# Kernel optimization log

Hardware: AMD Instinct MI355X
Metric: run time of the kernel (lower is better)

## Reference

```python
import jax, jax.numpy as jnp
from jax import lax
import numpy as np

PROPRIO = 48
NPTS = 1024
NP_PROX = 512
NP_DIST = 512
HP = 187  # proximal_feature_dim
HD = 64   # distal_feature_dim
B = 2048
NA = 12
ACTOR_DIMS = [PROPRIO + HP + HD, 1024, 512, 256, 128, NA]


def gru_last(x, wih, whh, bih, bhh):
    """torch-style GRU (gate order r,z,n), returns last hidden. x: [B,T,in]."""
    Bx, T, _ = x.shape
    H = whh.shape[1]
    gx = x @ wih.T + bih  # [B,T,3H], input projections precomputed
    def step(h, gxt):
        gh = h @ whh.T + bhh
        r = jax.nn.sigmoid(gxt[:, :H] + gh[:, :H])
        z = jax.nn.sigmoid(gxt[:, H:2 * H] + gh[:, H:2 * H])
        n = jnp.tanh(gxt[:, 2 * H:] + r * gh[:, 2 * H:])
        return (1.0 - z) * n + z * h, None
    h0 = jnp.zeros((Bx, H), x.dtype)
    hT, _ = lax.scan(step, h0, jnp.swapaxes(gx, 0, 1))
    return hT


def _encode(pts, w1, b1, w2, b2):
    h = jax.nn.elu(pts @ w1.T + b1)
    return jax.nn.elu(h @ w2.T + b2)


def _forward(obs, pe_prox_w1, pe_prox_b1, pe_prox_w2, pe_prox_b2,
             pe_dist_w1, pe_dist_b1, pe_dist_w2, pe_dist_b2,
             gru_prox_wih, gru_prox_whh, gru_prox_bih, gru_prox_bhh,
             gru_dist_wih, gru_dist_whh, gru_dist_bih, gru_dist_bhh,
             mem_prox_wih, mem_prox_whh, mem_prox_bih, mem_prox_bhh,
             mem_dist_wih, mem_dist_whh, mem_dist_bih, mem_dist_bhh,
             actor_w0, actor_b0, actor_w1, actor_b1, actor_w2, actor_b2,
             actor_w3, actor_b3, actor_w4, actor_b4,
             prox_idx, dist_idx):
    proprio = obs[:, :PROPRIO]
    lidar = obs[:, PROPRIO:].reshape(obs.shape[0], NPTS, 3)  # history_length=1
    # irregular gather of proximal/distal point subsets (sampling plan buffers)
    prox_enc = _encode(lidar[:, prox_idx], pe_prox_w1, pe_prox_b1, pe_prox_w2, pe_prox_b2)  # [B,512,64]
    dist_enc = _encode(lidar[:, dist_idx], pe_dist_w1, pe_dist_b1, pe_dist_w2, pe_dist_b2)  # [B,512,64]
    # spatial GRUs over the point sequence
    hp = gru_last(prox_enc, gru_prox_wih, gru_prox_whh, gru_prox_bih, gru_prox_bhh)  # [B,187]
    hd = gru_last(dist_enc, gru_dist_wih, gru_dist_whh, gru_dist_bih, gru_dist_bhh)  # [B,64]
    # temporal memory GRUs (single step, zero initial hidden)
    fp = gru_last(hp[:, None, :], mem_prox_wih, mem_prox_whh, mem_prox_bih, mem_prox_bhh)
    fd = gru_last(hd[:, None, :], mem_dist_wih, mem_dist_whh, mem_dist_bih, mem_dist_bhh)
    x = jnp.concatenate([proprio, fp, fd], axis=-1)  # [B,299]
    for w, b in ((actor_w0, actor_b0), (actor_w1, actor_b1), (actor_w2, actor_b2), (actor_w3, actor_b3)):
        x = jax.nn.elu(x @ w.T + b)
    return x @ actor_w4.T + actor_b4  # action mean [B,12]


def setup_inputs() -> dict:
    key = jax.random.key(0)
    ks = iter(jax.random.split(key, 64))
    def n(shape, scale=0.05):
        return (jax.random.normal(next(ks), shape, jnp.float32) * scale)
    inp = {}
    inp["obs"] = jax.random.normal(next(ks), (B, PROPRIO + NPTS * 3), jnp.float32)
    inp["prox_idx"] = jax.random.randint(next(ks), (NP_PROX,), 0, NPTS)
    inp["dist_idx"] = jax.random.randint(next(ks), (NP_DIST,), 0, NPTS)
    for pfx in ("pe_prox", "pe_dist"):
        inp[pfx + "_w1"] = n((64, 3)); inp[pfx + "_b1"] = jnp.zeros((64,), jnp.float32)
        inp[pfx + "_w2"] = n((64, 64)); inp[pfx + "_b2"] = jnp.zeros((64,), jnp.float32)
    for pfx, H, din in (("gru_prox", HP, 64), ("gru_dist", HD, 64), ("mem_prox", HP, HP), ("mem_dist", HD, HD)):
        inp[pfx + "_wih"] = n((3 * H, din)); inp[pfx + "_whh"] = n((3 * H, H))
        inp[pfx + "_bih"] = jnp.zeros((3 * H,), jnp.float32); inp[pfx + "_bhh"] = jnp.zeros((3 * H,), jnp.float32)
    for i, (di, do) in enumerate(zip(ACTOR_DIMS[:-1], ACTOR_DIMS[1:])):
        inp[f"actor_w{i}"] = n((do, di)); inp[f"actor_b{i}"] = jnp.zeros((do,), jnp.float32)
    return inp


def reference(obs, prox_idx, dist_idx,
              pe_prox_w1, pe_prox_b1, pe_prox_w2, pe_prox_b2,
              pe_dist_w1, pe_dist_b1, pe_dist_w2, pe_dist_b2,
              gru_prox_wih, gru_prox_whh, gru_prox_bih, gru_prox_bhh,
              gru_dist_wih, gru_dist_whh, gru_dist_bih, gru_dist_bhh,
              mem_prox_wih, mem_prox_whh, mem_prox_bih, mem_prox_bhh,
              mem_dist_wih, mem_dist_whh, mem_dist_bih, mem_dist_bhh,
              actor_w0, actor_b0, actor_w1, actor_b1, actor_w2, actor_b2,
              actor_w3, actor_b3, actor_w4, actor_b4):
    return _forward(obs, pe_prox_w1, pe_prox_b1, pe_prox_w2, pe_prox_b2,
                    pe_dist_w1, pe_dist_b1, pe_dist_w2, pe_dist_b2,
                    gru_prox_wih, gru_prox_whh, gru_prox_bih, gru_prox_bhh,
                    gru_dist_wih, gru_dist_whh, gru_dist_bih, gru_dist_bhh,
                    mem_prox_wih, mem_prox_whh, mem_prox_bih, mem_prox_bhh,
                    mem_dist_wih, mem_dist_whh, mem_dist_bih, mem_dist_bhh,
                    actor_w0, actor_b0, actor_w1, actor_b1, actor_w2, actor_b2,
                    actor_w3, actor_b3, actor_w4, actor_b4,
                    prox_idx, dist_idx)
```

## Files before the change

kernel.cpp:

```cpp
#include <hip/hip_runtime.h>
#include <stdint.h>

typedef __attribute__((ext_vector_type(8))) short short8;
typedef __attribute__((ext_vector_type(4))) float f32x4;
typedef __attribute__((ext_vector_type(4))) unsigned int u32x4;

#define DEV __device__ __forceinline__

#define L2E 1.4426950408889634f

DEV unsigned short f2bf(float f) {
    union { float f; uint32_t u; } v; v.f = f;
    return (unsigned short)((v.u + 0x7FFFu + ((v.u >> 16) & 1u)) >> 16);
}
#if defined(__has_builtin)
#if __has_builtin(__builtin_amdgcn_cvt_pk_bf16_f32)
#define HAS_PK_BF16 1
#endif
#endif
DEV uint32_t pk_bf16(float a, float b) {
#ifdef HAS_PK_BF16
    typedef __attribute__((ext_vector_type(2))) __bf16 bf2;
    union { bf2 v; uint32_t u; } cv;
    cv.v = __builtin_amdgcn_cvt_pk_bf16_f32(a, b);
    return cv.u;
#else
    return (uint32_t)f2bf(a) | ((uint32_t)f2bf(b) << 16);
#endif
}
DEV uint8_t f2fp8(float f) {
    union { float f; uint32_t u; } v; v.f = f;
    uint32_t s = (v.u >> 24) & 0x80u;
    uint32_t absu = v.u & 0x7FFFFFFFu;
    int E = (int)(absu >> 23);
    if (E >= 136) return (uint8_t)(s | 0x7E);
    if (E >= 121) {
        uint32_t m = absu & 0x7FFFFFu;
        uint32_t keep = m >> 20;
        uint32_t rest = m & 0xFFFFFu;
        uint32_t rnd = (rest > 0x80000u || (rest == 0x80000u && (keep & 1u))) ? 1u : 0u;
        uint32_t mag = (((uint32_t)(E - 120) << 3) | keep) + rnd;
        if (mag > 0x7Eu) mag = 0x7Eu;
        return (uint8_t)(s | mag);
    }
    float sc = __builtin_fabsf(f) * 512.f;
    uint32_t m8 = (uint32_t)(sc + 0.5f);
    if (m8 > 7u) return (uint8_t)(s | 0x08);
    return (uint8_t)(s | m8);
}
DEV float rcp1pe_(float x) {
    return __builtin_amdgcn_rcpf(1.f + __builtin_amdgcn_exp2f(x));
}
DEV float sig_(float x) { return rcp1pe_(-L2E * x); }
DEV float elu_(float x) {
    return x > 0.f ? x : __builtin_amdgcn_exp2f(L2E * x) - 1.f;
}
DEV f32x4 splat4(float v) { f32x4 r; r[0]=v; r[1]=v; r[2]=v; r[3]=v; return r; }
DEV void pin(short8& v) { asm volatile("" : "+v"(v)); }
DEV void pinl(long& v)  { asm volatile("" : "+v"(v)); }

struct PJob { const float* s; void* d; int Hs, NG, Ks, Kd, total; float s0, s1, s2; int fmt; };
struct PJobs { PJob j[13]; };

__global__ __launch_bounds__(256) void pack_all(PJobs P)
{
    PJob jb = P.j[blockIdx.y];
    int e = blockIdx.x * 256 + threadIdx.x;
    if (e >= jb.total) return;
    int n = e / jb.Kd, k = e - n * jb.Kd;
    int g = n / jb.NG, jj = n - g * jb.NG;
    float sc = (g == 0) ? jb.s0 : ((g == 1) ? jb.s1 : jb.s2);
    float v = (jj < jb.Hs && k < jb.Ks) ? jb.s[(size_t)(g * jb.Hs + jj) * jb.Ks + k] * sc : 0.f;
    if (jb.fmt) ((uint8_t*)jb.d)[e] = f2fp8(v);
    else        ((unsigned short*)jb.d)[e] = f2bf(v);
}

__global__ __launch_bounds__(256) void enc_kernel(
    const float* __restrict__ obs, const int* __restrict__ idx,
    const float* __restrict__ w1, const float* __restrict__ b1,
    const unsigned short* __restrict__ w2p, const float* __restrict__ b2,
    uint8_t* __restrict__ enc8)
{
    const int b = blockIdx.x, t0 = blockIdx.y * 64;
    const int tid = threadIdx.x;
    __shared__ __align__(16) float pts[64][4];
    __shared__ float w1s[256];
    __shared__ float b1s[64], b2s[64];
    __shared__ __align__(16) unsigned short h1s[64][72];

    if (tid < 192) w1s[(tid/3)*4 + (tid - (tid/3)*3)] = w1[tid];
    if (tid < 64) { b1s[tid] = b1[tid]; b2s[tid] = b2[tid]; }
    for (int e = tid; e < 192; e += 256) {
        int p = e / 3, c2 = e - p * 3;
        int pi = idx[t0 + p];
        pts[p][c2] = obs[(size_t)b * 3120 + 48 + (size_t)pi * 3 + c2];
    }
    __syncthreads();
#pragma unroll
    for (int r = 0; r < 16; ++r) {
        int e = tid + r * 256;
        int p = e >> 6, ch = e & 63;
        float v = w1s[ch*4]*pts[p][0] + w1s[ch*4+1]*pts[p][1]
                + w1s[ch*4+2]*pts[p][2] + b1s[ch];
        h1s[p][ch] = f2bf(elu_(v));
    }
    __syncthreads();
    const int wave = tid >> 6, lane = tid & 63, quad = lane >> 4, l16 = lane & 15;
#pragma unroll
    for (int ct = 0; ct < 4; ++ct) {
        f32x4 a2 = splat4(0.f);
#pragma unroll
        for (int ks = 0; ks < 2; ++ks) {
            short8 af = *(const short8*)(&h1s[wave*16 + l16][ks*32 + quad*8]);
            short8 bf = *(const short8*)(w2p + (ct*16 + l16)*64 + ks*32 + quad*8);
            a2 = __builtin_amdgcn_mfma_f32_16x16x32_bf16(af, bf, a2, 0, 0, 0);
        }
        int c = ct*16 + l16;
        float b2v = b2s[c];
#pragma unroll
        for (int j = 0; j < 4; ++j) {
            int m = wave*16 + quad*4 + j;
            enc8[((size_t)b*512 + t0 + m)*64 + c] = f2fp8(elu_(a2[j] + b2v));
        }
    }
}

DEV void gru_body_pre(int blk, const uint8_t* __restrict__ enc8,
                      const uint8_t* __restrict__ wih8,
                      const unsigned short* __restrict__ whh,
                      const float* __restrict__ bih, const float* __restrict__ bhh,
                      unsigned short* __restrict__ houtb, char* smem)
{
    constexpr int H = 187, KP = 192, KS = 6, HP8 = 200;
    unsigned short* hlds = (unsigned short*)smem;
    uint8_t* xs = (uint8_t*)(smem + 12800);

    const int tid  = threadIdx.x;
    const int wave = tid >> 6, lane = tid & 63, quad = lane >> 4, l16 = lane & 15;
    const int b0   = blk * 16;
    const int c    = wave * 16 + l16;

    for (int e = tid; e < 2*16*HP8; e += 768) hlds[e] = 0;

    short8 whr[3][KS];
    long   wx8[3][2];
#pragma unroll
    for (int g = 0; g < 3; ++g) {
#pragma unroll
        for (int ks = 0; ks < KS; ++ks)
            whr[g][ks] = *(const short8*)(whh + ((size_t)(g*KP + c))*KP + ks*32 + quad*8);
#pragma unroll
        for (int ks = 0; ks < 2; ++ks)
            wx8[g][ks] = *(const long*)(wih8 + ((size_t)(g*KP + c))*64 + ks*32 + quad*8);
    }
#pragma unroll
    for (int g = 0; g < 3; ++g) {
#pragma unroll
        for (int ks = 0; ks < KS; ++ks) pin(whr[g][ks]);
#pragma unroll
        for (int ks = 0; ks < 2; ++ks)  pinl(wx8[g][ks]);
    }
    float bsr = 0.f, bsz = 0.f, binx = 0.f, bhnn = 0.f;
    if (c < H) {
        bsr  = -L2E * (bih[c]       + bhh[c]);
        bsz  = -L2E * (bih[H + c]   + bhh[H + c]);
        binx = 2.f * L2E * bih[2*H + c];
        bhnn = 2.f * L2E * bhh[2*H + c];
    }
    float hreg[4] = {0.f, 0.f, 0.f, 0.f};

    u32x4 xq;
    const int xrow = lane >> 2, xseg = lane & 3;
    if (wave == 0) {
        xq = *(const u32x4*)(enc8 + ((size_t)(b0 + xrow)*512 + 0)*64 + xseg*16);
        *(u32x4*)(xs + 0*1280 + xrow*80 + xseg*16) = xq;
        xq = *(const u32x4*)(enc8 + ((size_t)(b0 + xrow)*512 + 1)*64 + xseg*16);
    }
    __syncthreads();

    int cur = 0;
    for (int t = 0; t < 512; ++t) {
        if (wave == 0) {
            *(u32x4*)(xs + ((t+1)&1)*1280 + xrow*80 + xseg*16) = xq;
            int tn = (t + 2 < 512) ? t + 2 : 511;
            xq = *(const u32x4*)(enc8 + ((size_t)(b0 + xrow)*512 + tn)*64 + xseg*16);
        }
        const uint8_t* xsr = xs + (t&1)*1280;
        const unsigned short* hc = hlds + cur * (16*HP8);
        unsigned short*       hn = hlds + (cur ^ 1) * (16*HP8);

        f32x4 acc[4];
        acc[0] = splat4(bsr);
        acc[1] = splat4(bsz);
        acc[2] = splat4(binx);
        acc[3] = splat4(bhnn);
#pragma unroll
        for (int ks = 0; ks < 2; ++ks) {
            long a8 = *(const long*)(xsr + l16*80 + ks*32 + quad*8);
            acc[0] = __builtin_amdgcn_mfma_f32_16x16x32_fp8_fp8(a8, wx8[0][ks], acc[0], 0, 0, 0);
            acc[1] = __builtin_amdgcn_mfma_f32_16x16x32_fp8_fp8(a8, wx8[1][ks], acc[1], 0, 0, 0);
            acc[2] = __builtin_amdgcn_mfma_f32_16x16x32_fp8_fp8(a8, wx8[2][ks], acc[2], 0, 0, 0);
        }
#pragma unroll
        for (int ks = 0; ks < KS; ++ks) {
            short8 ah = *(const short8*)(hc + l16*HP8 + ks*32 + quad*8);
            acc[0] = __builtin_amdgcn_mfma_f32_16x16x32_bf16(ah, whr[0][ks], acc[0], 0, 0, 0);
            acc[1] = __builtin_amdgcn_mfma_f32_16x16x32_bf16(ah, whr[1][ks], acc[1], 0, 0, 0);
            acc[3] = __builtin_amdgcn_mfma_f32_16x16x32_bf16(ah, whr[2][ks], acc[3], 0, 0, 0);
        }
        float hv[4];
#pragma unroll
        for (int j = 0; j < 4; ++j) {
            float r  = rcp1pe_(acc[0][j]);
            float zg = rcp1pe_(acc[1][j]);
            float nn = __builtin_fmaf(-2.f, rcp1pe_(__builtin_fmaf(r, acc[3][j], acc[2][j])), 1.f);
            hv[j] = __builtin_fmaf(zg, hreg[j] - nn, nn);
            hreg[j] = hv[j];
        }
        uint32_t p01 = pk_bf16(hv[0], hv[1]);
        uint32_t p23 = pk_bf16(hv[2], hv[3]);
        hn[(quad*4+0)*HP8 + c] = (unsigned short)p01;
        hn[(quad*4+1)*HP8 + c] = (unsigned short)(p01 >> 16);
        hn[(quad*4+2)*HP8 + c] = (unsigned short)p23;
        hn[(quad*4+3)*HP8 + c] = (unsigned short)(p23 >> 16);
        cur ^= 1;
        __syncthreads();
    }
#pragma unroll
    for (int j = 0; j < 4; ++j) {
        int m = quad*4 + j;
        houtb[(size_t)(b0 + m)*KP + c] = (c < H) ? f2bf(hreg[j]) : 0;
    }
}

template<int H, int KP>
DEV void gru_body_fused(int blk,
                  const float* __restrict__ obs, const int* __restrict__ idx,
                  const float* __restrict__ w1, const float* __restrict__ b1,
                  const float* __restrict__ w2, const float* __restrict__ b2,
                  const unsigned short* __restrict__ wih, const unsigned short* __restrict__ whh,
                  const float* __restrict__ bih, const float* __restrict__ bhh,
                  unsigned short* __restrict__ houtb, char* smem)
{
    constexpr int NCT = KP / 16;
    constexpr int KS  = KP / 32;
    constexpr int HP8 = KP + 8;

    unsigned short* hlds = (unsigned short*)(smem);
    unsigned short* xs   = (unsigned short*)(smem + 12800);
    unsigned short* h1s  = (unsigned short*)(smem + 17408);
    unsigned short* w2s  = (unsigned short*)(smem + 22016);
    float* ptsb          = (float*)(smem + 31232);
    float* w1s           = (float*)(smem + 31744);
    float* b1s           = (float*)(smem + 32768);
    float* b2s           = (float*)(smem + 33024);

    const int tid  = threadIdx.x;
    const int wave = tid >> 6, lane = tid & 63, quad = lane >> 4, l16 = lane & 15;
    const int b0   = blk * 16;
    const int ct   = wave;
    const bool act = (ct < NCT);
    const int c    = ct * 16 + l16;

    for (int e = tid; e < 2*16*HP8; e += 768) hlds[e] = 0;
    for (int e = tid; e < 4096; e += 768) { int n = e >> 6, k = e & 63; w2s[n*72 + k] = f2bf(w2[e]); }
    if (tid < 192) w1s[(tid/3)*4 + (tid - (tid/3)*3)] = w1[tid];
    if (tid < 64) { b1s[tid] = b1[tid]; b2s[tid] = b2[tid]; }

    const float* myrow = obs + (size_t)(b0 + (tid & 15)) * 3120 + 48;
    float px = 0.f, py = 0.f, pz = 0.f;
    if (tid < 16) {
        int p0 = idx[0];
        ptsb[tid*4 + 0] = myrow[3*p0 + 0];
        ptsb[tid*4 + 1] = myrow[3*p0 + 1];
        ptsb[tid*4 + 2] = myrow[3*p0 + 2];
        int p1 = idx[1];
        px = myrow[3*p1 + 0]; py = myrow[3*p1 + 1]; pz = myrow[3*p1 + 2];
    }

    short8 whr[3][KS];
    short8 wxr[3][2];
    float bsr = 0.f, bsz = 0.f, binx = 0.f, bhnn = 0.f;
    {
        const int cl = act ? c : l16;
#pragma unroll
        for (int g = 0; g < 3; ++g) {
#pragma unroll
            for (int ks = 0; ks < KS; ++ks)
                whr[g][ks] = *(const short8*)(whh + ((size_t)(g*KP + cl))*KP + ks*32 + quad*8);
#pragma unroll
            for (int ks = 0; ks < 2; ++ks)
                wxr[g][ks] = *(const short8*)(wih + ((size_t)(g*KP + cl))*64 + ks*32 + quad*8);
        }
    }
#pragma unroll
    for (int g = 0; g < 3; ++g) {
#pragma unroll
        for (int ks = 0; ks < KS; ++ks) pin(whr[g][ks]);
#pragma unroll
        for (int ks = 0; ks < 2; ++ks)  pin(wxr[g][ks]);
    }
    if (act && c < H) {
        bsr  = -L2E * (bih[c]       + bhh[c]);
        bsz  = -L2E * (bih[H + c]   + bhh[H + c]);
        binx = 2.f * L2E * bih[2*H + c];
        bhnn = 2.f * L2E * bhh[2*H + c];
    }
    float hreg[4] = {0.f, 0.f, 0.f, 0.f};

    __syncthreads();

    int cur = 0;
    for (int i = 0; i < 514; ++i) {
        if (i < 512) {
            const float* pt = ptsb + (i & 1) * 64;
            unsigned short* h1w = h1s + (i & 1) * (16*72);
#pragma unroll
            for (int e = tid; e < 1024; e += 768) {
                int p = e >> 6, ch = e & 63;
                float v = w1s[ch*4+0]*pt[p*4+0] + w1s[ch*4+1]*pt[p*4+1]
                        + w1s[ch*4+2]*pt[p*4+2] + b1s[ch];
                h1w[p*72 + ch] = f2bf(elu_(v));
            }
            if (tid < 16) {
                float* dst = ptsb + ((i+1) & 1) * 64 + tid*4;
                dst[0] = px; dst[1] = py; dst[2] = pz;
                int tn = (i + 2 < 512) ? i + 2 : 511;
                int pn = idx[tn];
                px = myrow[3*pn + 0]; py = myrow[3*pn + 1]; pz = myrow[3*pn + 2];
            }
        }
        if (i >= 1 && i < 513 && wave < 4) {
            const unsigned short* h1r = h1s + ((i-1) & 1) * (16*72);
            unsigned short*       xw  = xs  + ((i-1) & 1) * (16*72);
            f32x4 a2 = splat4(0.f);
#pragma unroll
            for (int ks = 0; ks < 2; ++ks) {
                short8 af = *(const short8*)(h1r + l16*72 + ks*32 + quad*8);
                short8 bf = *(const short8*)(w2s + (wave*16 + l16)*72 + ks*32 + quad*8);
                a2 = __builtin_amdgcn_mfma_f32_16x16x32_bf16(af, bf, a2, 0, 0, 0);
            }
            int c2 = wave*16 + l16;
            float b2v = b2s[c2];
#pragma unroll
            for (int j = 0; j < 4; ++j)
                xw[(quad*4 + j)*72 + c2] = f2bf(elu_(a2[j] + b2v));
        }
        if (i >= 2) {
            int t = i - 2;
            const unsigned short* xsr = xs + (t & 1) * (16*72);
            const unsigned short* hc  = hlds + cur * (16*HP8);
            unsigned short*       hn  = hlds + (cur ^ 1) * (16*HP8);
            if (act) {
                f32x4 acc[4];
                acc[0] = splat4(bsr);
                acc[1] = splat4(bsz);
                acc[2] = splat4(binx);
                acc[3] = splat4(bhnn);
#pragma unroll
                for (int ks = 0; ks < 2; ++ks) {
                    short8 xf = *(const short8*)(xsr + l16*72 + ks*32 + quad*8);
                    acc[0] = __builtin_amdgcn_mfma_f32_16x16x32_bf16(xf, wxr[0][ks], acc[0], 0, 0, 0);
                    acc[1] = __builtin_amdgcn_mfma_f32_16x16x32_bf16(xf, wxr[1][ks], acc[1], 0, 0, 0);
                    acc[2] = __builtin_amdgcn_mfma_f32_16x16x32_bf16(xf, wxr[2][ks], acc[2], 0, 0, 0);
                }
#pragma unroll
                for (int ks = 0; ks < KS; ++ks) {
                    short8 ah = *(const short8*)(hc + l16*HP8 + ks*32 + quad*8);
                    acc[0] = __builtin_amdgcn_mfma_f32_16x16x32_bf16(ah, whr[0][ks], acc[0], 0, 0, 0);
                    acc[1] = __builtin_amdgcn_mfma_f32_16x16x32_bf16(ah, whr[1][ks], acc[1], 0, 0, 0);
                    acc[3] = __builtin_amdgcn_mfma_f32_16x16x32_bf16(ah, whr[2][ks], acc[3], 0, 0, 0);
                }
                float hv[4];
#pragma unroll
                for (int j = 0; j < 4; ++j) {
                    float r  = rcp1pe_(acc[0][j]);
                    float zg = rcp1pe_(acc[1][j]);
                    float nn = __builtin_fmaf(-2.f, rcp1pe_(__builtin_fmaf(r, acc[3][j], acc[2][j])), 1.f);
                    hv[j] = __builtin_fmaf(zg, hreg[j] - nn, nn);
                    hreg[j] = hv[j];
                }
                uint32_t p01 = pk_bf16(hv[0], hv[1]);
                uint32_t p23 = pk_bf16(hv[2], hv[3]);
                hn[(quad*4+0)*HP8 + c] = (unsigned short)p01;
                hn[(quad*4+1)*HP8 + c] = (unsigned short)(p01 >> 16);
                hn[(quad*4+2)*HP8 + c] = (unsigned short)p23;
                hn[(quad*4+3)*HP8 + c] = (unsigned short)(p23 >> 16);
            }
            cur ^= 1;
        }
        __syncthreads();
    }

    if (act)
#pragma unroll
        for (int j = 0; j < 4; ++j) {
            int m = quad*4 + j;
            houtb[(size_t)(b0 + m)*KP + c] = (c < H) ? f2bf(hreg[j]) : 0;
        }
}

__global__ __launch_bounds__(768) void gru_kernel(
    int mode,
    const float* __restrict__ obs,
    const int* __restrict__ prox_idx, const int* __restrict__ dist_idx,
    const uint8_t* __restrict__ encp8, const uint8_t* __restrict__ wihp8,
    const float* __restrict__ w1p, const float* __restrict__ b1p,
    const float* __restrict__ w2p, const float* __restrict__ b2p,
    const float* __restrict__ w1d, const float* __restrict__ b1d,
    const float* __restrict__ w2d, const float* __restrict__ b2d,
    const unsigned short* __restrict__ wihp, const unsigned short* __restrict__ whhp,
    const unsigned short* __restrict__ wihd, const unsigned short* __restrict__ whhd,
    const float* __restrict__ bihp, const float* __restrict__ bhhp,
    const float* __restrict__ bihd, const float* __restrict__ bhhd,
    unsigned short* __restrict__ hpb, unsigned short* __restrict__ hdb)
{
    __shared__ __align__(16) char smem[33280];
    if (blockIdx.x < 128) {
        if (mode == 0)
            gru_body_pre(blockIdx.x, encp8, wihp8, whhp, bihp, bhhp, hpb, smem);
        else
            gru_body_fused<187, 192>(blockIdx.x, obs, prox_idx, w1p, b1p, w2p, b2p,
                                     wihp, whhp, bihp, bhhp, hpb, smem);
    } else {
        gru_body_fused<64, 64>(blockIdx.x - 128, obs, dist_idx, w1d, b1d, w2d, b2d,
                               wihd, whhd, bihd, bhhd, hdb, smem);
    }
}

__global__ __launch_bounds__(256) void memfuse_kernel(
    const float* __restrict__ obs,
    const unsigned short* __restrict__ hpb, const unsigned short* __restrict__ hdb,
    const unsigned short* __restrict__ mwp, const unsigned short* __restrict__ mwd,
    const float* __restrict__ mbip, const float* __restrict__ mbhp,
    const float* __restrict__ mbid, const float* __restrict__ mbhd,
    unsigned short* __restrict__ x0b)
{
    __shared__ __align__(16) unsigned short Asl[64*40];
    __shared__ __align__(16) unsigned short Bsl[3][64*40];
    const int tid = threadIdx.x;
    const int wave = tid >> 6, lane = tid & 63, quad = lane >> 4, l16 = lane & 15;
    const int z = blockIdx.x, m0 = blockIdx.y * 64;
    const bool isp = (z < 3);
    const unsigned short* A = isp ? hpb : hdb;
    const unsigned short* B = isp ? mwp : mwd;
    const float* bi = isp ? mbip : mbid;
    const float* bh = isp ? mbhp : mbhd;
    const int Kp = isp ? 192 : 64;
    const int Hh = isp ? 187 : 64;
    const int jb = isp ? z * 64 : 0;
    const int cbase = isp ? 48 : 235;
    const int r = tid >> 2, sg = (tid & 3) * 8;

    f32x4 acc[3][4];
#pragma unroll
    for (int g = 0; g < 3; ++g)
#pragma unroll
        for (int nt = 0; nt < 4; ++nt) acc[g][nt] = splat4(0.f);

    for (int k0 = 0; k0 < Kp; k0 += 32) {
        *(short8*)(Asl + r*40 + sg) = *(const short8*)(A + (size_t)(m0 + r)*Kp + k0 + sg);
#pragma unroll
        for (int g = 0; g < 3; ++g)
            *(short8*)(Bsl[g] + r*40 + sg) =
                *(const short8*)(B + (size_t)(g*Kp + jb + r)*Kp + k0 + sg);
        __syncthreads();
        short8 af = *(const short8*)(Asl + (wave*16 + l16)*40 + quad*8);
#pragma unroll
        for (int g = 0; g < 3; ++g)
#pragma unroll
            for (int nt = 0; nt < 4; ++nt) {
                short8 bf = *(const short8*)(Bsl[g] + (nt*16 + l16)*40 + quad*8);
                acc[g][nt] = __builtin_amdgcn_mfma_f32_16x16x32_bf16(af, bf, acc[g][nt], 0, 0, 0);
            }
        __syncthreads();
    }
#pragma unroll
    for (int nt = 0; nt < 4; ++nt) {
        int j = jb + nt*16 + l16;
        bool valid = (j < Hh);
        float br = 0.f, bz = 0.f, bnx = 0.f, bnh = 0.f;
        if (valid) {
            br  = -L2E * (bi[j] + bh[j]);
            bz  = -L2E * (bi[Hh + j] + bh[Hh + j]);
            bnx = 2.f * L2E * bi[2*Hh + j];
            bnh = 2.f * L2E * bh[2*Hh + j];
        }
#pragma unroll
        for (int jj = 0; jj < 4; ++jj) {
            int m = m0 + wave*16 + quad*4 + jj;
            float rr = rcp1pe_(acc[0][nt][jj] + br);
            float zz = rcp1pe_(acc[1][nt][jj] + bz);
            float tt = __builtin_fmaf(rr, bnh, acc[2][nt][jj] + bnx);
            float nn = __builtin_fmaf(-2.f, rcp1pe_(tt), 1.f);
            float v  = (1.f - zz) * nn;
            if (valid) x0b[(size_t)m*320 + cbase + j] = f2bf(v);
        }
    }
    if (z == 0) {
        for (int e = tid; e < 64*48; e += 256) {
            int m = m0 + e / 48, cc = e - (e / 48) * 48;
            x0b[(size_t)m*320 + cc] = f2bf(obs[(size_t)m*3120 + cc]);
        }
    }
    if (z == 3) {
        for (int e = tid; e < 64*21; e += 256) {
            int m = m0 + e / 21, cc = 299 + (e - (e / 21) * 21);
            x0b[(size_t)m*320 + cc] = 0;
        }
    }
}

__global__ __launch_bounds__(256) void bgemm_kernel(
    const unsigned short* __restrict__ A, const unsigned short* __restrict__ B,
    const float* __restrict__ bias, void* __restrict__ C,
    int Kp, int Np, int Nstore, int mode)
{
    __shared__ __align__(16) unsigned short Asl[64*40];
    __shared__ __align__(16) unsigned short Bsl[64*40];
    const int tid = threadIdx.x;
    const int wave = tid >> 6, lane = tid & 63, quad = lane >> 4, l16 = lane & 15;
    const int n0 = blockIdx.x * 64, m0 = blockIdx.y * 64;
    const int r = tid >> 2, sg = (tid & 3) * 8;

    f32x4 acc[4];
#pragma unroll
    for (int nt = 0; nt < 4; ++nt) acc[nt] = splat4(0.f);

    for (int k0 = 0; k0 < Kp; k0 += 32) {
        short8 av = *(const short8*)(A + (size_t)(m0 + r)*Kp + k0 + sg);
        short8 bv;
        if (n0 + r < Np) bv = *(const short8*)(B + (size_t)(n0 + r)*Kp + k0 + sg);
        else { short8 zz; for (int q = 0; q < 8; ++q) zz[q] = 0; bv = zz; }
        *(short8*)(Asl + r*40 + sg) = av;
        *(short8*)(Bsl + r*40 + sg) = bv;
        __syncthreads();
        short8 af = *(const short8*)(Asl + (wave*16 + l16)*40 + quad*8);
#pragma unroll
        for (int nt = 0; nt < 4; ++nt) {
            short8 bf = *(const short8*)(Bsl + (nt*16 + l16)*40 + quad*8);
            acc[nt] = __builtin_amdgcn_mfma_f32_16x16x32_bf16(af, bf, acc[nt], 0, 0, 0);
        }
        __syncthreads();
    }
#pragma unroll
    for (int nt = 0; nt < 4; ++nt) {
        int n = n0 + nt*16 + l16;
        float bv = (bias && n < Np) ? bias[n] : 0.f;
#pragma unroll
        for (int j = 0; j < 4; ++j) {
            int m = m0 + wave*16 + quad*4 + j;
            float v = acc[nt][j] + bv;
            if (mode == 1) {
                ((unsigned short*)C)[(size_t)m*Np + n] = f2bf(elu_(v));
            } else {
                if (n < Nstore) ((float*)C)[(size_t)m*Nstore + n] = v;
            }
        }
    }
}

extern "C" void kernel_launch(void* const* d_in, const int* in_sizes, int n_in,
                              void* d_out, int out_size, void* d_ws, size_t ws_size,
                              hipStream_t stream)
{
    (void)in_sizes; (void)n_in; (void)out_size;
    const float* obs        = (const float*)d_in[0];
    const int*   prox_idx   = (const int*)d_in[1];
    const int*   dist_idx   = (const int*)d_in[2];
    const float* pe_prox_w1 = (const float*)d_in[3];
    const float* pe_prox_b1 = (const float*)d_in[4];
    const float* pe_prox_w2 = (const float*)d_in[5];
    const float* pe_prox_b2 = (const float*)d_in[6];
    const float* pe_dist_w1 = (const float*)d_in[7];
    const float* pe_dist_b1 = (const float*)d_in[8];
    const float* pe_dist_w2 = (const float*)d_in[9];
    const float* pe_dist_b2 = (const float*)d_in[10];
    const float* gp_wih = (const float*)d_in[11];
    const float* gp_whh = (const float*)d_in[12];
    const float* gp_bih = (const float*)d_in[13];
    const float* gp_bhh = (const float*)d_in[14];
    const float* gd_wih = (const float*)d_in[15];
    const float* gd_whh = (const float*)d_in[16];
    const float* gd_bih = (const float*)d_in[17];
    const float* gd_bhh = (const float*)d_in[18];
    const float* mp_wih = (const float*)d_in[19];
    const float* mp_bih = (const float*)d_in[21];
    const float* mp_bhh = (const float*)d_in[22];
    const float* md_wih = (const float*)d_in[23];
    const float* md_bih = (const float*)d_in[25];
    const float* md_bhh = (const float*)d_in[26];
    const float* aw0 = (const float*)d_in[27]; const float* ab0 = (const float*)d_in[28];
    const float* aw1 = (const float*)d_in[29]; const float* ab1 = (const float*)d_in[30];
    const float* aw2 = (const float*)d_in[31]; const float* ab2 = (const float*)d_in[32];
    const float* aw3 = (const float*)d_in[33]; const float* ab3 = (const float*)d_in[34];
    const float* aw4 = (const float*)d_in[35]; const float* ab4 = (const float*)d_in[36];
    float* out = (float*)d_out;

    char* ws = (char*)d_ws;
    size_t off = 0;
    auto alloc = [&](size_t bytes) -> char* {
        char* p = ws + off;
        off = (off + bytes + 255) & ~(size_t)255;
        return p;
    };
    unsigned short* wih_p = (unsigned short*)alloc(36864*2);
    unsigned short* whh_p = (unsigned short*)alloc(110592*2);
    unsigned short* wih_d = (unsigned short*)alloc(12288*2);
    unsigned short* whh_d = (unsigned short*)alloc(12288*2);
    unsigned short* mw_p  = (unsigned short*)alloc(110592*2);
    unsigned short* mw_d  = (unsigned short*)alloc(12288*2);
    unsigned short* w0p   = (unsigned short*)alloc((size_t)1024*320*2);
    unsigned short* w1p   = (unsigned short*)alloc((size_t)512*1024*2);
    unsigned short* w2p   = (unsigned short*)alloc((size_t)256*512*2);
    unsigned short* w3p   = (unsigned short*)alloc((size_t)128*256*2);
    unsigned short* w4p   = (unsigned short*)alloc((size_t)16*128*2);
    unsigned short* w2e   = (unsigned short*)alloc(4096*2);
    uint8_t* wih8         = (uint8_t*)alloc(576*64);
    unsigned short* hpb   = (unsigned short*)alloc((size_t)2048*192*2);
    unsigned short* hdb   = (unsigned short*)alloc((size_t)2048*64*2);
    unsigned short* x0b   = (unsigned short*)alloc((size_t)2048*320*2);
    unsigned short* a1b   = (unsigned short*)alloc((size_t)2048*1024*2);
    unsigned short* a2b   = (unsigned short*)alloc((size_t)2048*512*2);
    unsigned short* a3b   = (unsigned short*)alloc((size_t)2048*256*2);
    unsigned short* a4b   = (unsigned short*)alloc((size_t)2048*128*2);
    uint8_t* enc8         = (uint8_t*)alloc((size_t)2048*512*64);
    const int mode = (off <= ws_size) ? 0 : 1;

    const float SR = -L2E, SN = 2.f * L2E;
    PJobs P;
    P.j[0]  = { gp_wih, wih_p, 187, 192, 64, 64, 36864, SR, SR, SN, 0 };
    P.j[1]  = { gp_whh, whh_p, 187, 192, 187, 192, 110592, SR, SR, SN, 0 };
    P.j[2]  = { gd_wih, wih_d, 64, 64, 64, 64, 12288, SR, SR, SN, 0 };
    P.j[3]  = { gd_whh, whh_d, 64, 64, 64, 64, 12288, SR, SR, SN, 0 };
    P.j[4]  = { mp_wih, mw_p, 187, 192, 187, 192, 110592, SR, SR, SN, 0 };
    P.j[5]  = { md_wih, mw_d, 64, 64, 64, 64, 12288, SR, SR, SN, 0 };
    P.j[6]  = { aw0, w0p, 1024, 1024, 299, 320, 327680, 1.f, 1.f, 1.f, 0 };
    P.j[7]  = { aw1, w1p, 512, 512, 1024, 1024, 524288, 1.f, 1.f, 1.f, 0 };
    P.j[8]  = { aw2, w2p, 256, 256, 512, 512, 131072, 1.f, 1.f, 1.f, 0 };
    P.j[9]  = { aw3, w3p, 128, 128, 256, 256, 32768, 1.f, 1.f, 1.f, 0 };
    P.j[10] = { aw4, w4p, 12, 16, 128, 128, 2048, 1.f, 1.f, 1.f, 0 };
    P.j[11] = { pe_prox_w2, w2e, 64, 64, 64, 64, 4096, 1.f, 1.f, 1.f, 0 };
    P.j[12] = { gp_wih, wih8, 187, 192, 64, 64, 36864, SR, SR, SN, 1 };
    pack_all<<<dim3(2048, 13), 256, 0, stream>>>(P);

    if (mode == 0) {
        enc_kernel<<<dim3(2048, 8), 256, 0, stream>>>(
            obs, prox_idx, pe_prox_w1, pe_prox_b1, w2e, pe_prox_b2, enc8);
    }

    gru_kernel<<<256, 768, 0, stream>>>(
        mode, obs, prox_idx, dist_idx, enc8, wih8,
        pe_prox_w1, pe_prox_b1, pe_prox_w2, pe_prox_b2,
        pe_dist_w1, pe_dist_b1, pe_dist_w2, pe_dist_b2,
        wih_p, whh_p, wih_d, whh_d,
        gp_bih, gp_bhh, gd_bih, gd_bhh, hpb, hdb);

    memfuse_kernel<<<dim3(4, 32), 256, 0, stream>>>(
        obs, hpb, hdb, mw_p, mw_d, mp_bih, mp_bhh, md_bih, md_bhh, x0b);

    bgemm_kernel<<<dim3(16, 32), 256, 0, stream>>>(x0b, w0p, ab0, a1b, 320, 1024, 1024, 1);
    bgemm_kernel<<<dim3(8,  32), 256, 0, stream>>>(a1b, w1p, ab1, a2b, 1024, 512, 512, 1);
    bgemm_kernel<<<dim3(4,  32), 256, 0, stream>>>(a2b, w2p, ab2, a3b, 512, 256, 256, 1);
    bgemm_kernel<<<dim3(2,  32), 256, 0, stream>>>(a3b, w3p, ab3, a4b, 256, 128, 128, 1);
    bgemm_kernel<<<dim3(1,  32), 256, 0, stream>>>(a4b, w4p, ab4, out, 128, 16, 12, 0);
}
```

Measured before the change: 811.0 us.

## Vectorize FP8 packing, swizzle GRU LDS, widen GEMM K-tile, fuse last two layers

Uses the hardware packed FP8 conversion and stages encoder outputs in shared memory so they can be written with 16-byte stores. Applies an XOR swizzle to the GRU hidden-state LDS layout to cut bank conflicts. Doubles the bgemm K step to 64 to halve the number of barriers. Fuses actor layers 3 and 4 into one kernel, which removes the a4 intermediate and one launch. The hardware FP8 conversion may round slightly differently from the software f2fp8, and the fused kernel runs only 32 blocks.

```diff
diff --git a/kernel.cpp b/kernel.cpp
--- a/kernel.cpp
+++ b/kernel.cpp
@@ -16,6 +16,9 @@
 #if defined(__has_builtin)
 #if __has_builtin(__builtin_amdgcn_cvt_pk_bf16_f32)
 #define HAS_PK_BF16 1
+#endif
+#if __has_builtin(__builtin_amdgcn_cvt_pk_fp8_f32)
+#define HAS_PK_FP8 1
 #endif
 #endif
 DEV uint32_t pk_bf16(float a, float b) {
@@ -48,6 +51,16 @@
     if (m8 > 7u) return (uint8_t)(s | 0x08);
     return (uint8_t)(s | m8);
 }
+DEV uint32_t pk_fp8x4(float a, float b, float c, float d) {
+#ifdef HAS_PK_FP8
+    int lo   = __builtin_amdgcn_cvt_pk_fp8_f32(a, b, 0, false);
+    int both = __builtin_amdgcn_cvt_pk_fp8_f32(c, d, lo, true);
+    return (uint32_t)both;
+#else
+    return (uint32_t)f2fp8(a) | ((uint32_t)f2fp8(b) << 8)
+         | ((uint32_t)f2fp8(c) << 16) | ((uint32_t)f2fp8(d) << 24);
+#endif
+}
 DEV float rcp1pe_(float x) {
     return __builtin_amdgcn_rcpf(1.f + __builtin_amdgcn_exp2f(x));
 }
@@ -71,7 +84,7 @@
     int g = n / jb.NG, jj = n - g * jb.NG;
     float sc = (g == 0) ? jb.s0 : ((g == 1) ? jb.s1 : jb.s2);
     float v = (jj < jb.Hs && k < jb.Ks) ? jb.s[(size_t)(g * jb.Hs + jj) * jb.Ks + k] * sc : 0.f;
-    if (jb.fmt) ((uint8_t*)jb.d)[e] = f2fp8(v);
+    if (jb.fmt) ((uint8_t*)jb.d)[e] = (uint8_t)(pk_fp8x4(v, 0.f, 0.f, 0.f) & 0xFFu);
     else        ((unsigned short*)jb.d)[e] = f2bf(v);
 }
 
@@ -87,6 +100,7 @@
     __shared__ float w1s[256];
     __shared__ float b1s[64], b2s[64];
     __shared__ __align__(16) unsigned short h1s[64][72];
+    __shared__ __align__(16) uint8_t x8s[64 * 80];
 
     if (tid < 192) w1s[(tid/3)*4 + (tid - (tid/3)*3)] = w1[tid];
     if (tid < 64) { b1s[tid] = b1[tid]; b2s[tid] = b2[tid]; }
@@ -117,11 +131,17 @@
         }
         int c = ct*16 + l16;
         float b2v = b2s[c];
-#pragma unroll
-        for (int j = 0; j < 4; ++j) {
-            int m = wave*16 + quad*4 + j;
-            enc8[((size_t)b*512 + t0 + m)*64 + c] = f2fp8(elu_(a2[j] + b2v));
-        }
+        uint32_t pk = pk_fp8x4(elu_(a2[0] + b2v), elu_(a2[1] + b2v),
+                               elu_(a2[2] + b2v), elu_(a2[3] + b2v));
+#pragma unroll
+        for (int j = 0; j < 4; ++j)
+            x8s[(wave*16 + quad*4 + j)*80 + c] = (uint8_t)(pk >> (8*j));
+    }
+    __syncthreads();
+    {
+        int row = tid >> 2, seg = tid & 3;
+        *(u32x4*)(enc8 + ((size_t)b*512 + t0 + row)*64 + seg*16) =
+            *(const u32x4*)(x8s + row*80 + seg*16);
     }
 }
 
@@ -139,6 +159,11 @@
     const int wave = tid >> 6, lane = tid & 63, quad = lane >> 4, l16 = lane & 15;
     const int b0   = blk * 16;
     const int c    = wave * 16 + l16;
+
+    const int sx = (l16 >> 2) & 3;
+    const int qo = (quad ^ sx) * 8;
+    const int cc = c >> 3, cl = c & 7;
+    const int wcol = ((cc & ~3) | ((cc & 3) ^ quad)) * 8 + cl;
 
     for (int e = tid; e < 2*16*HP8; e += 768) hlds[e] = 0;
 
@@ -203,7 +228,7 @@
         }
 #pragma unroll
         for (int ks = 0; ks < KS; ++ks) {
-            short8 ah = *(const short8*)(hc + l16*HP8 + ks*32 + quad*8);
+            short8 ah = *(const short8*)(hc + l16*HP8 + ks*32 + qo);
             acc[0] = __builtin_amdgcn_mfma_f32_16x16x32_bf16(ah, whr[0][ks], acc[0], 0, 0, 0);
             acc[1] = __builtin_amdgcn_mfma_f32_16x16x32_bf16(ah, whr[1][ks], acc[1], 0, 0, 0);
             acc[3] = __builtin_amdgcn_mfma_f32_16x16x32_bf16(ah, whr[2][ks], acc[3], 0, 0, 0);
@@ -219,10 +244,10 @@
         }
         uint32_t p01 = pk_bf16(hv[0], hv[1]);
         uint32_t p23 = pk_bf16(hv[2], hv[3]);
-        hn[(quad*4+0)*HP8 + c] = (unsigned short)p01;
-        hn[(quad*4+1)*HP8 + c] = (unsigned short)(p01 >> 16);
-        hn[(quad*4+2)*HP8 + c] = (unsigned short)p23;
-        hn[(quad*4+3)*HP8 + c] = (unsigned short)(p23 >> 16);
+        hn[(quad*4+0)*HP8 + wcol] = (unsigned short)p01;
+        hn[(quad*4+1)*HP8 + wcol] = (unsigned short)(p01 >> 16);
+        hn[(quad*4+2)*HP8 + wcol] = (unsigned short)p23;
+        hn[(quad*4+3)*HP8 + wcol] = (unsigned short)(p23 >> 16);
         cur ^= 1;
         __syncthreads();
     }
@@ -516,30 +541,37 @@
     const float* __restrict__ bias, void* __restrict__ C,
     int Kp, int Np, int Nstore, int mode)
 {
-    __shared__ __align__(16) unsigned short Asl[64*40];
-    __shared__ __align__(16) unsigned short Bsl[64*40];
+    __shared__ __align__(16) unsigned short Asl[64*72];
+    __shared__ __align__(16) unsigned short Bsl[64*72];
     const int tid = threadIdx.x;
     const int wave = tid >> 6, lane = tid & 63, quad = lane >> 4, l16 = lane & 15;
     const int n0 = blockIdx.x * 64, m0 = blockIdx.y * 64;
-    const int r = tid >> 2, sg = (tid & 3) * 8;
+    const int r = tid >> 2, sg = (tid & 3) * 16;
 
     f32x4 acc[4];
 #pragma unroll
     for (int nt = 0; nt < 4; ++nt) acc[nt] = splat4(0.f);
 
-    for (int k0 = 0; k0 < Kp; k0 += 32) {
-        short8 av = *(const short8*)(A + (size_t)(m0 + r)*Kp + k0 + sg);
-        short8 bv;
-        if (n0 + r < Np) bv = *(const short8*)(B + (size_t)(n0 + r)*Kp + k0 + sg);
-        else { short8 zz; for (int q = 0; q < 8; ++q) zz[q] = 0; bv = zz; }
-        *(short8*)(Asl + r*40 + sg) = av;
-        *(short8*)(Bsl + r*40 + sg) = bv;
+    for (int k0 = 0; k0 < Kp; k0 += 64) {
+        *(short8*)(Asl + r*72 + sg)     = *(const short8*)(A + (size_t)(m0 + r)*Kp + k0 + sg);
+        *(short8*)(Asl + r*72 + sg + 8) = *(const short8*)(A + (size_t)(m0 + r)*Kp + k0 + sg + 8);
+        if (n0 + r < Np) {
+            *(short8*)(Bsl + r*72 + sg)     = *(const short8*)(B + (size_t)(n0 + r)*Kp + k0 + sg);
+            *(short8*)(Bsl + r*72 + sg + 8) = *(const short8*)(B + (size_t)(n0 + r)*Kp + k0 + sg + 8);
+        } else {
+            short8 zz; for (int q = 0; q < 8; ++q) zz[q] = 0;
+            *(short8*)(Bsl + r*72 + sg) = zz;
+            *(short8*)(Bsl + r*72 + sg + 8) = zz;
+        }
         __syncthreads();
-        short8 af = *(const short8*)(Asl + (wave*16 + l16)*40 + quad*8);
-#pragma unroll
-        for (int nt = 0; nt < 4; ++nt) {
-            short8 bf = *(const short8*)(Bsl + (nt*16 + l16)*40 + quad*8);
-            acc[nt] = __builtin_amdgcn_mfma_f32_16x16x32_bf16(af, bf, acc[nt], 0, 0, 0);
+#pragma unroll
+        for (int ks = 0; ks < 2; ++ks) {
+            short8 af = *(const short8*)(Asl + (wave*16 + l16)*72 + ks*32 + quad*8);
+#pragma unroll
+            for (int nt = 0; nt < 4; ++nt) {
+                short8 bf = *(const short8*)(Bsl + (nt*16 + l16)*72 + ks*32 + quad*8);
+                acc[nt] = __builtin_amdgcn_mfma_f32_16x16x32_bf16(af, bf, acc[nt], 0, 0, 0);
+            }
         }
         __syncthreads();
     }
@@ -557,6 +589,73 @@
                 if (n < Nstore) ((float*)C)[(size_t)m*Nstore + n] = v;
             }
         }
+    }
+}
+
+__global__ __launch_bounds__(256) void gemm34_kernel(
+    const unsigned short* __restrict__ A,
+    const unsigned short* __restrict__ W3,
+    const float* __restrict__ b3,
+    const unsigned short* __restrict__ W4,
+    const float* __restrict__ b4,
+    float* __restrict__ out)
+{
+    __shared__ __align__(16) char smem[9216 + 18432];
+    unsigned short* Asl  = (unsigned short*)smem;
+    unsigned short* B3sl = (unsigned short*)(smem + 9216);
+    unsigned short* a4s  = (unsigned short*)smem;
+    const int tid = threadIdx.x;
+    const int wave = tid >> 6, lane = tid & 63, quad = lane >> 4, l16 = lane & 15;
+    const int m0 = blockIdx.x * 64;
+
+    f32x4 acc3[8];
+#pragma unroll
+    for (int nt = 0; nt < 8; ++nt) acc3[nt] = splat4(0.f);
+
+    const int r = tid >> 2, sg = (tid & 3) * 16;
+    const int r2 = tid >> 1, sg2 = (tid & 1) * 32;
+    for (int k0 = 0; k0 < 256; k0 += 64) {
+        *(short8*)(Asl + r*72 + sg)     = *(const short8*)(A + (size_t)(m0 + r)*256 + k0 + sg);
+        *(short8*)(Asl + r*72 + sg + 8) = *(const short8*)(A + (size_t)(m0 + r)*256 + k0 + sg + 8);
+#pragma unroll
+        for (int s = 0; s < 4; ++s)
+            *(short8*)(B3sl + r2*72 + sg2 + s*8) =
+                *(const short8*)(W3 + (size_t)r2*256 + k0 + sg2 + s*8);
+        __syncthreads();
+#pragma unroll
+        for (int ks = 0; ks < 2; ++ks) {
+            short8 af = *(const short8*)(Asl + (wave*16 + l16)*72 + ks*32 + quad*8);
+#pragma unroll
+            for (int nt = 0; nt < 8; ++nt) {
+                short8 bf = *(const short8*)(B3sl + (nt*16 + l16)*72 + ks*32 + quad*8);
+                acc3[nt] = __builtin_amdgcn_mfma_f32_16x16x32_bf16(af, bf, acc3[nt], 0, 0, 0);
+            }
+        }
+        __syncthreads();
+    }
+#pragma unroll
+    for (int nt = 0; nt < 8; ++nt) {
+        int n = nt*16 + l16;
+        float bv = b3[n];
+#pragma unroll
+        for (int j = 0; j < 4; ++j) {
+            int m = wave*16 + quad*4 + j;
+            a4s[m*136 + n] = f2bf(elu_(acc3[nt][j] + bv));
+        }
+    }
+    __syncthreads();
+    f32x4 acc4 = splat4(0.f);
+#pragma unroll
+    for (int ks = 0; ks < 4; ++ks) {
+        short8 af = *(const short8*)(a4s + (wave*16 + l16)*136 + ks*32 + quad*8);
+        short8 bf = *(const short8*)(W4 + (size_t)l16*128 + ks*32 + quad*8);
+        acc4 = __builtin_amdgcn_mfma_f32_16x16x32_bf16(af, bf, acc4, 0, 0, 0);
+    }
+    if (l16 < 12) {
+        float bv = b4[l16];
+#pragma unroll
+        for (int j = 0; j < 4; ++j)
+            out[(size_t)(m0 + wave*16 + quad*4 + j)*12 + l16] = acc4[j] + bv;
     }
 }
 
@@ -623,7 +722,6 @@
     unsigned short* a1b   = (unsigned short*)alloc((size_t)2048*1024*2);
     unsigned short* a2b   = (unsigned short*)alloc((size_t)2048*512*2);
     unsigned short* a3b   = (unsigned short*)alloc((size_t)2048*256*2);
-    unsigned short* a4b   = (unsigned short*)alloc((size_t)2048*128*2);
     uint8_t* enc8         = (uint8_t*)alloc((size_t)2048*512*64);
     const int mode = (off <= ws_size) ? 0 : 1;
 
@@ -662,6 +760,5 @@
     bgemm_kernel<<<dim3(16, 32), 256, 0, stream>>>(x0b, w0p, ab0, a1b, 320, 1024, 1024, 1);
     bgemm_kernel<<<dim3(8,  32), 256, 0, stream>>>(a1b, w1p, ab1, a2b, 1024, 512, 512, 1);
     bgemm_kernel<<<dim3(4,  32), 256, 0, stream>>>(a2b, w2p, ab2, a3b, 512, 256, 256, 1);
-    bgemm_kernel<<<dim3(2,  32), 256, 0, stream>>>(a3b, w3p, ab3, a4b, 256, 128, 128, 1);
-    bgemm_kernel<<<dim3(1,  32), 256, 0, stream>>>(a4b, w4p, ab4, out, 128, 16, 12, 0);
-}
+    gemm34_kernel<<<32, 256, 0, stream>>>(a3b, w3p, ab3, w4p, ab4, out);
+}
```

Result: no change. 805.3 us (-0.7%).
